# Kernel optimization log

Measured on AMD Instinct MI355X. Metric: run time of the kernel, lower is better.

The kernel has to match this reference:

```python
import jax, jax.numpy as jnp
import numpy as np

N_NODES = 100000
N_EDGES = 1600000
IN_FEATS = 128
N_HIDDEN = 128
OUT_DIM = 32
BN_EPS = 1e-5


def setup_inputs() -> dict:
    key = jax.random.key(0)
    ks = jax.random.split(key, 12)
    s = 0.05  # weight init scale
    return {
        "features": jax.random.normal(ks[0], (N_NODES, IN_FEATS), dtype=jnp.float32),
        "src": jax.random.randint(ks[1], (N_EDGES,), 0, N_NODES),
        "dst": jax.random.randint(ks[2], (N_EDGES,), 0, N_NODES),
        # layer 0: in_feats -> n_hidden
        "Ws0": jax.random.normal(ks[3], (IN_FEATS, N_HIDDEN), dtype=jnp.float32) * s,
        "Wn0": jax.random.normal(ks[4], (IN_FEATS, N_HIDDEN), dtype=jnp.float32) * s,
        "b0": jnp.zeros((N_HIDDEN,), jnp.float32),
        # layer 1: n_hidden -> n_hidden
        "Ws1": jax.random.normal(ks[5], (N_HIDDEN, N_HIDDEN), dtype=jnp.float32) * s,
        "Wn1": jax.random.normal(ks[6], (N_HIDDEN, N_HIDDEN), dtype=jnp.float32) * s,
        "b1": jnp.zeros((N_HIDDEN,), jnp.float32),
        # layer 2 (output): n_hidden -> out_dim, no activation
        "Ws2": jax.random.normal(ks[7], (N_HIDDEN, OUT_DIM), dtype=jnp.float32) * s,
        "Wn2": jax.random.normal(ks[8], (N_HIDDEN, OUT_DIM), dtype=jnp.float32) * s,
        "b2": jnp.zeros((OUT_DIM,), jnp.float32),
        # batch norms after layers 0 and 1
        "g0": jnp.ones((N_HIDDEN,), jnp.float32),
        "be0": jnp.zeros((N_HIDDEN,), jnp.float32),
        "g1": jnp.ones((N_HIDDEN,), jnp.float32),
        "be1": jnp.zeros((N_HIDDEN,), jnp.float32),
    }


def _sage_mean(h, src, dst, inv_deg, Ws, Wn, b):
    # DGL SAGEConv('mean'): fc_self(h) + fc_neigh(mean of in-neighbor feats)
    agg = jax.ops.segment_sum(h[src], dst, num_segments=N_NODES) * inv_deg
    return h @ Ws + agg @ Wn + b


def _batch_norm(h, gamma, beta):
    mu = jnp.mean(h, axis=0)
    var = jnp.var(h, axis=0)
    return (h - mu) * jax.lax.rsqrt(var + BN_EPS) * gamma + beta


def reference(features, src, dst, Ws0, Wn0, b0, Ws1, Wn1, b1, Ws2, Wn2, b2, g0, be0, g1, be1):
    ones = jnp.ones((N_EDGES,), jnp.float32)
    deg = jax.ops.segment_sum(ones, dst, num_segments=N_NODES)
    inv_deg = (1.0 / jnp.maximum(deg, 1.0))[:, None]  # [N,1]

    # layer 0: SAGEConv internal activation, then BN + external activation
    h = jax.nn.relu(_sage_mean(features, src, dst, inv_deg, Ws0, Wn0, b0))
    h = jax.nn.relu(_batch_norm(h, g0, be0))
    # layer 1 (hidden)
    h = jax.nn.relu(_sage_mean(h, src, dst, inv_deg, Ws1, Wn1, b1))
    h = jax.nn.relu(_batch_norm(h, g1, be1))
    # layer 2 (output): no activation, no BN (idx > n_hidden_layers)
    h = _sage_mean(h, src, dst, inv_deg, Ws2, Wn2, b2)

    # dgl.mean_nodes over a single graph -> [1, out_dim], then softmax over classes
    hg = jnp.mean(h, axis=0, keepdims=True)
    return jax.nn.softmax(hg, axis=1)
```

## Files before the change

### kernel.cpp

```cpp
#include <hip/hip_runtime.h>
#include <hip/hip_bf16.h>

typedef __hip_bfloat16 bf16;
typedef __hip_bfloat162 bf162;

#define NN 100000
#define NE 1600000
#define BN_EPS 1e-5f

#define BSH 8
#define NBUCK ((NN + 255) >> BSH)
#define ABLK 128
#define EPBA ((NE + ABLK - 1) / ABLK)
#define CAP 6144

struct alignas(16) bf16x8 { bf16 v[8]; };

typedef __bf16 bfrag __attribute__((ext_vector_type(8)));
typedef float f4 __attribute__((ext_vector_type(4)));
typedef float f2 __attribute__((ext_vector_type(2)));

static __device__ __forceinline__ float b2f(bf16 x){ return __bfloat162float(x); }
static __device__ __forceinline__ bf16 f2b(float x){ return __float2bfloat16(x); }

static __device__ __forceinline__ uint2 pk8_fp8(float x0,float x1,float x2,float x3,
                                                float x4,float x5,float x6,float x7)
{
    int lo = __builtin_amdgcn_cvt_pk_fp8_f32(x0, x1, 0, 0);
    lo = __builtin_amdgcn_cvt_pk_fp8_f32(x2, x3, lo, 1);
    int hi = __builtin_amdgcn_cvt_pk_fp8_f32(x4, x5, 0, 0);
    hi = __builtin_amdgcn_cvt_pk_fp8_f32(x6, x7, hi, 1);
    return make_uint2((unsigned)lo, (unsigned)hi);
}

__global__ __launch_bounds__(256) void k_convert(const float* __restrict__ in,
                                                 unsigned char* __restrict__ outf8, int n)
{
    int i = (blockIdx.x * 256 + threadIdx.x) * 8;
    if (i + 7 < n) {
        float4 a = *(const float4*)(in + i);
        float4 b = *(const float4*)(in + i + 4);
        *(uint2*)(outf8 + i) = pk8_fp8(a.x,a.y,a.z,a.w,b.x,b.y,b.z,b.w);
    }
}

__global__ __launch_bounds__(256) void k_wtrans(const float* __restrict__ W0, const float* __restrict__ W1,
                                                const float* __restrict__ W2, const float* __restrict__ W3,
                                                bf16* __restrict__ T0, bf16* __restrict__ T1,
                                                bf16* __restrict__ T2, bf16* __restrict__ T3)
{
    int m = blockIdx.x >> 6;
    int t = (blockIdx.x & 63) * 256 + threadIdx.x;
    const float* W = (m == 0) ? W0 : (m == 1) ? W1 : (m == 2) ? W2 : W3;
    bf16* T = (m == 0) ? T0 : (m == 1) ? T1 : (m == 2) ? T2 : T3;
    int n = t >> 7, k = t & 127;
    T[n * 128 + k] = f2b(W[k * 128 + n]);
}

__global__ __launch_bounds__(256) void k_pa1(const int* __restrict__ dst, const int* __restrict__ src,
                                             int* __restrict__ bucketCountD, int* __restrict__ blockBaseD,
                                             int* __restrict__ bucketCountS, int* __restrict__ blockBaseS)
{
    __shared__ int histD[NBUCK];
    __shared__ int histS[NBUCK];
    int t = threadIdx.x;
    for (int i = t; i < NBUCK; i += 256) { histD[i] = 0; histS[i] = 0; }
    __syncthreads();
    int e0 = blockIdx.x * EPBA, e1 = min(e0 + EPBA, NE);
    for (int e = e0 + t; e < e1; e += 256) {
        unsigned bd = ((unsigned)dst[e]) >> BSH;
        unsigned bs = ((unsigned)src[e]) >> BSH;
        if (bd < (unsigned)NBUCK) atomicAdd(&histD[bd], 1);
        if (bs < (unsigned)NBUCK) atomicAdd(&histS[bs], 1);
    }
    __syncthreads();
    for (int i = t; i < NBUCK; i += 256) {
        blockBaseD[blockIdx.x * NBUCK + i] = atomicAdd(&bucketCountD[i], histD[i]);
        blockBaseS[blockIdx.x * NBUCK + i] = atomicAdd(&bucketCountS[i], histS[i]);
    }
}

__global__ __launch_bounds__(512) void k_bscan2(const int* __restrict__ cntD, int* __restrict__ startD,
                                                const int* __restrict__ cntS, int* __restrict__ startS)
{
    __shared__ int sd[512];
    const int* cnt = (blockIdx.x == 0) ? cntD : cntS;
    int* start = (blockIdx.x == 0) ? startD : startS;
    int t = threadIdx.x;
    int v = (t < NBUCK) ? cnt[t] : 0;
    sd[t] = v;
    __syncthreads();
    for (int o = 1; o < 512; o <<= 1) {
        int x = (t >= o) ? sd[t - o] : 0;
        __syncthreads();
        sd[t] += x;
        __syncthreads();
    }
    if (t < NBUCK) start[t] = sd[t] - v;
    if (t == 0) start[NBUCK] = NE;
}

__global__ __launch_bounds__(256) void k_pa2(const int* __restrict__ src, const int* __restrict__ dst,
                                             const int* __restrict__ bucketStartD, const int* __restrict__ blockBaseD,
                                             const int* __restrict__ bucketStartS, const int* __restrict__ blockBaseS,
                                             unsigned* __restrict__ packD, unsigned* __restrict__ packS)
{
    __shared__ int baseD[NBUCK];
    __shared__ int curD[NBUCK];
    __shared__ int baseS[NBUCK];
    __shared__ int curS[NBUCK];
    int t = threadIdx.x;
    for (int i = t; i < NBUCK; i += 256) {
        baseD[i] = bucketStartD[i] + blockBaseD[blockIdx.x * NBUCK + i];
        curD[i] = 0;
        baseS[i] = bucketStartS[i] + blockBaseS[blockIdx.x * NBUCK + i];
        curS[i] = 0;
    }
    __syncthreads();
    int e0 = blockIdx.x * EPBA, e1 = min(e0 + EPBA, NE);
    for (int e = e0 + t; e < e1; e += 256) {
        int s = src[e], d = dst[e];
        unsigned bd = ((unsigned)d) >> BSH;
        if (bd < (unsigned)NBUCK) {
            int r = atomicAdd(&curD[bd], 1);
            unsigned idx = (unsigned)(baseD[bd] + r);
            if (idx < (unsigned)NE)
                packD[idx] = (((unsigned)d & 255u) << 24) | ((unsigned)s & 0xFFFFFFu);
        }
        unsigned bs = ((unsigned)s) >> BSH;
        if (bs < (unsigned)NBUCK) {
            int r = atomicAdd(&curS[bs], 1);
            unsigned idx = (unsigned)(baseS[bs] + r);
            if (idx < (unsigned)NE)
                packS[idx] = (((unsigned)s & 255u) << 24) | ((unsigned)d & 0xFFFFFFu);
        }
    }
}

__global__ __launch_bounds__(256) void k_pbD(const unsigned* __restrict__ packD, const int* __restrict__ bucketStartD,
                                             int* __restrict__ offs, float* __restrict__ invd,
                                             int* __restrict__ esrc)
{
    __shared__ int dcnt[256];
    __shared__ int sscan[256];
    __shared__ int cur[256];
    __shared__ int S[CAP];
    int t = threadIdx.x;
    int b = blockIdx.x;
    int base = b << BSH;
    dcnt[t] = 0;
    cur[t] = 0;
    for (int i = t; i < CAP; i += 256) S[i] = 0;
    __syncthreads();
    int p0 = bucketStartD[b], p1 = bucketStartD[b + 1];
    int cnt = p1 - p0;
    for (int i = p0 + t; i < p1; i += 256)
        atomicAdd(&dcnt[packD[i] >> 24], 1);
    __syncthreads();
    int my = dcnt[t];
    sscan[t] = my;
    __syncthreads();
    for (int o = 1; o < 256; o <<= 1) {
        int v = (t >= o) ? sscan[t - o] : 0;
        __syncthreads();
        sscan[t] += v;
        __syncthreads();
    }
    int lo = sscan[t] - my;
    if (base + t < NN) {
        offs[base + t] = p0 + lo;
        invd[base + t] = 1.0f / (float)max(my, 1);
    }
    if (b == NBUCK - 1 && t == 0) offs[NN] = NE;
    __syncthreads();
    sscan[t] = lo;
    __syncthreads();
    if (cnt <= CAP) {
        for (int i = p0 + t; i < p1; i += 256) {
            unsigned v = packD[i];
            unsigned li = v >> 24;
            int pos = sscan[li] + atomicAdd(&cur[li], 1);
            if ((unsigned)pos >= (unsigned)cnt) pos = cnt - 1;
            S[pos] = (int)(v & 0xFFFFFFu);
        }
        __syncthreads();
        for (int i = t; i < cnt; i += 256) esrc[p0 + i] = S[i];
    } else {
        for (int i = p0 + t; i < p1; i += 256) {
            unsigned v = packD[i];
            unsigned li = v >> 24;
            int pos = sscan[li] + atomicAdd(&cur[li], 1);
            if ((unsigned)pos >= (unsigned)cnt) pos = cnt - 1;
            esrc[p0 + pos] = (int)(v & 0xFFFFFFu);
        }
    }
}

__global__ __launch_bounds__(256) void k_wsrc2(const unsigned* __restrict__ packS, const int* __restrict__ bucketStartS,
                                               const float* __restrict__ invd, float* __restrict__ wsrc)
{
    __shared__ float wacc[256];
    int t = threadIdx.x;
    wacc[t] = 0.f;
    __syncthreads();
    int b = blockIdx.x;
    int base = b << BSH;
    int p0 = bucketStartS[b], p1 = bucketStartS[b + 1];
    for (int i = p0 + t; i < p1; i += 256) {
        unsigned v = packS[i];
        unsigned li = v >> 24;
        unsigned dy = v & 0xFFFFFFu;
        if (dy >= (unsigned)NN) dy = 0u;
        atomicAdd(&wacc[li], invd[dy]);
    }
    __syncthreads();
    if (base + t < NN) wsrc[base + t] = wacc[t];
}

__global__ __launch_bounds__(256) void k_aggregate(const unsigned char* __restrict__ inf8, bf16* __restrict__ out,
                                                   const int* __restrict__ offs, const int* __restrict__ esrc,
                                                   const float* __restrict__ invd,
                                                   const float* __restrict__ scsh, int use_ss)
{
    int row = blockIdx.x * 4 + (threadIdx.x >> 6);
    if (row >= NN) return;
    int lane = threadIdx.x & 63;
    int grp = lane >> 4;
    int c0 = (lane & 15) * 8;
    float sc[8], sh[8];
    if (use_ss) {
#pragma unroll
        for (int j = 0; j < 8; j++) { sc[j] = scsh[c0 + j]; sh[j] = scsh[128 + c0 + j]; }
    }
    int e0 = offs[row], e1 = offs[row + 1];
    float a[8];
#pragma unroll
    for (int j = 0; j < 8; j++) a[j] = 0.f;

    auto unpack = [&](uint2 u, float* v) {
        f2 p0 = __builtin_amdgcn_cvt_pk_f32_fp8(u.x, 0);
        f2 p1 = __builtin_amdgcn_cvt_pk_f32_fp8(u.x, 1);
        f2 p2 = __builtin_amdgcn_cvt_pk_f32_fp8(u.y, 0);
        f2 p3 = __builtin_amdgcn_cvt_pk_f32_fp8(u.y, 1);
        v[0]=p0.x; v[1]=p0.y; v[2]=p1.x; v[3]=p1.y; v[4]=p2.x; v[5]=p2.y; v[6]=p3.x; v[7]=p3.y;
    };

    int e = e0 + grp;
    for (; e + 12 < e1; e += 16) {
        int s0 = esrc[e], s1 = esrc[e + 4], s2 = esrc[e + 8], s3 = esrc[e + 12];
        uint2 u0 = *(const uint2*)&inf8[(size_t)s0 * 128 + c0];
        uint2 u1 = *(const uint2*)&inf8[(size_t)s1 * 128 + c0];
        uint2 u2 = *(const uint2*)&inf8[(size_t)s2 * 128 + c0];
        uint2 u3 = *(const uint2*)&inf8[(size_t)s3 * 128 + c0];
        float v0[8], v1[8], v2[8], v3[8];
        unpack(u0, v0); unpack(u1, v1); unpack(u2, v2); unpack(u3, v3);
        if (use_ss) {
#pragma unroll
            for (int j = 0; j < 8; j++)
                a[j] += fmaxf(v0[j] * sc[j] + sh[j], 0.f) + fmaxf(v1[j] * sc[j] + sh[j], 0.f)
                      + fmaxf(v2[j] * sc[j] + sh[j], 0.f) + fmaxf(v3[j] * sc[j] + sh[j], 0.f);
        } else {
#pragma unroll
            for (int j = 0; j < 8; j++)
                a[j] += (v0[j] + v1[j]) + (v2[j] + v3[j]);
        }
    }
    if (e < e1) {
        int i1 = e + 4, i2 = e + 8;
        float m1 = (i1 < e1) ? 1.f : 0.f;
        float m2 = (i2 < e1) ? 1.f : 0.f;
        if (i1 >= e1) i1 = e;
        if (i2 >= e1) i2 = e;
        int s0 = esrc[e], s1 = esrc[i1], s2 = esrc[i2];
        uint2 u0 = *(const uint2*)&inf8[(size_t)s0 * 128 + c0];
        uint2 u1 = *(const uint2*)&inf8[(size_t)s1 * 128 + c0];
        uint2 u2 = *(const uint2*)&inf8[(size_t)s2 * 128 + c0];
        float v0[8], v1[8], v2[8];
        unpack(u0, v0); unpack(u1, v1); unpack(u2, v2);
        if (use_ss) {
#pragma unroll
            for (int j = 0; j < 8; j++)
                a[j] += fmaxf(v0[j] * sc[j] + sh[j], 0.f)
                      + m1 * fmaxf(v1[j] * sc[j] + sh[j], 0.f)
                      + m2 * fmaxf(v2[j] * sc[j] + sh[j], 0.f);
        } else {
#pragma unroll
            for (int j = 0; j < 8; j++)
                a[j] += v0[j] + m1 * v1[j] + m2 * v2[j];
        }
    }
#pragma unroll
    for (int j = 0; j < 8; j++) {
        a[j] += __shfl_xor(a[j], 16);
        a[j] += __shfl_xor(a[j], 32);
    }
    if (grp == 0) {
        float id = invd[row];
        bf16x8 o;
#pragma unroll
        for (int j = 0; j < 8; j++) o.v[j] = f2b(a[j] * id);
        *(bf16x8*)&out[(size_t)row * 128 + c0] = o;
    }
}

#define GM 128
__global__ __launch_bounds__(256) void k_gemm_mfma(const void* __restrict__ HsSrc, int hs_fp8,
                                                   const bf16* __restrict__ Ag,
                                                   const bf16* __restrict__ Wst, const bf16* __restrict__ Wnt,
                                                   const float* __restrict__ bias,
                                                   const float* __restrict__ scsh, int use_ss,
                                                   bf16* __restrict__ outp, unsigned char* __restrict__ outf8,
                                                   float* __restrict__ bnsums)
{
    __shared__ bf16 smem[2][128][72];
    __shared__ float sredsum[128], sredsq[128];
    int t = threadIdx.x;
    int row0 = blockIdx.x * GM;
    int lane = t & 63;
    int l16 = lane & 15;
    int quad = lane >> 4;
    int m0w = (t >> 6) * 32;

    if (t < 128) { sredsum[t] = 0.f; sredsq[t] = 0.f; }

    f4 acc[2][8];
#pragma unroll
    for (int rt = 0; rt < 2; rt++)
#pragma unroll
        for (int ct = 0; ct < 8; ct++) { f4 z = {0.f, 0.f, 0.f, 0.f}; acc[rt][ct] = z; }

    for (int kc = 0; kc < 128; kc += 64) {
#pragma unroll
        for (int i = 0; i < 4; i++) {
            int f = i * 256 + t;
            int row = f >> 3;
            int col8 = (f & 7) * 8;
            int grow = row0 + row;
            float hv32[8];
            bf16x8 av;
            if (grow < NN) {
                if (hs_fp8) {
                    uint2 u = *(const uint2*)((const unsigned char*)HsSrc + (size_t)grow * 128 + kc + col8);
                    f2 q0 = __builtin_amdgcn_cvt_pk_f32_fp8(u.x, 0);
                    f2 q1 = __builtin_amdgcn_cvt_pk_f32_fp8(u.x, 1);
                    f2 q2 = __builtin_amdgcn_cvt_pk_f32_fp8(u.y, 0);
                    f2 q3 = __builtin_amdgcn_cvt_pk_f32_fp8(u.y, 1);
                    hv32[0]=q0.x; hv32[1]=q0.y; hv32[2]=q1.x; hv32[3]=q1.y;
                    hv32[4]=q2.x; hv32[5]=q2.y; hv32[6]=q3.x; hv32[7]=q3.y;
                } else {
                    const float* fp = (const float*)HsSrc + (size_t)grow * 128 + kc + col8;
                    float4 x = *(const float4*)fp;
                    float4 y = *(const float4*)(fp + 4);
                    hv32[0]=x.x; hv32[1]=x.y; hv32[2]=x.z; hv32[3]=x.w;
                    hv32[4]=y.x; hv32[5]=y.y; hv32[6]=y.z; hv32[7]=y.w;
                }
                av = *(const bf16x8*)&Ag[(size_t)grow * 128 + kc + col8];
            } else {
#pragma unroll
                for (int j = 0; j < 8; j++) { hv32[j] = 0.f; av.v[j] = f2b(0.f); }
            }
            if (use_ss) {
#pragma unroll
                for (int j = 0; j < 8; j++) {
                    int k = kc + col8 + j;
                    hv32[j] = fmaxf(hv32[j] * scsh[k] + scsh[128 + k], 0.f);
                }
            }
            bf16x8 hv;
#pragma unroll
            for (int j = 0; j < 8; j++) hv.v[j] = f2b(hv32[j]);
            *(bf16x8*)&smem[0][row][col8] = hv;
            *(bf16x8*)&smem[1][row][col8] = av;
        }
        __syncthreads();
#pragma unroll
        for (int ks2 = 0; ks2 < 2; ks2++) {
            int ko = ks2 * 32 + quad * 8;
            bfrag ah0 = *(const bfrag*)&smem[0][m0w + l16][ko];
            bfrag ah1 = *(const bfrag*)&smem[0][m0w + 16 + l16][ko];
            bfrag aa0 = *(const bfrag*)&smem[1][m0w + l16][ko];
            bfrag aa1 = *(const bfrag*)&smem[1][m0w + 16 + l16][ko];
            int kg = kc + ks2 * 32 + quad * 8;
#pragma unroll
            for (int ct = 0; ct < 8; ct++) {
                bfrag bs  = *(const bfrag*)&Wst[(ct * 16 + l16) * 128 + kg];
                bfrag bnf = *(const bfrag*)&Wnt[(ct * 16 + l16) * 128 + kg];
                acc[0][ct] = __builtin_amdgcn_mfma_f32_16x16x32_bf16(ah0, bs,  acc[0][ct], 0, 0, 0);
                acc[0][ct] = __builtin_amdgcn_mfma_f32_16x16x32_bf16(aa0, bnf, acc[0][ct], 0, 0, 0);
                acc[1][ct] = __builtin_amdgcn_mfma_f32_16x16x32_bf16(ah1, bs,  acc[1][ct], 0, 0, 0);
                acc[1][ct] = __builtin_amdgcn_mfma_f32_16x16x32_bf16(aa1, bnf, acc[1][ct], 0, 0, 0);
            }
        }
        __syncthreads();
    }

    bf16 (*sout)[136] = (bf16(*)[136])&smem[0][0][0];
    float psum[8], psq[8];
#pragma unroll
    for (int ct = 0; ct < 8; ct++) {
        float bv = bias[ct * 16 + l16];
        float s = 0.f, s2 = 0.f;
#pragma unroll
        for (int rt = 0; rt < 2; rt++) {
#pragma unroll
            for (int r = 0; r < 4; r++) {
                int lrow = m0w + rt * 16 + quad * 4 + r;
                float v = fmaxf(acc[rt][ct][r] + bv, 0.f);
                sout[lrow][ct * 16 + l16] = f2b(v);
                if (row0 + lrow < NN) { s += v; s2 += v * v; }
            }
        }
        psum[ct] = s; psq[ct] = s2;
    }
#pragma unroll
    for (int ct = 0; ct < 8; ct++) {
        psum[ct] += __shfl_xor(psum[ct], 16); psum[ct] += __shfl_xor(psum[ct], 32);
        psq[ct]  += __shfl_xor(psq[ct], 16);  psq[ct]  += __shfl_xor(psq[ct], 32);
    }
    if (lane < 16) {
#pragma unroll
        for (int ct = 0; ct < 8; ct++) {
            atomicAdd(&sredsum[ct * 16 + lane], psum[ct]);
            atomicAdd(&sredsq[ct * 16 + lane],  psq[ct]);
        }
    }
    __syncthreads();
#pragma unroll
    for (int i = 0; i < 8; i++) {
        int f = i * 256 + t;
        int row = f >> 4;
        int c16 = f & 15;
        int grow = row0 + row;
        if (grow < NN) {
            bf16x8 ov = *(const bf16x8*)&sout[row][c16 * 8];
            if (outp) *(bf16x8*)&outp[(size_t)grow * 128 + c16 * 8] = ov;
            if (outf8) {
                *(uint2*)&outf8[(size_t)grow * 128 + c16 * 8] =
                    pk8_fp8(b2f(ov.v[0]), b2f(ov.v[1]), b2f(ov.v[2]), b2f(ov.v[3]),
                            b2f(ov.v[4]), b2f(ov.v[5]), b2f(ov.v[6]), b2f(ov.v[7]));
            }
        }
    }
    if (t < 128) {
        atomicAdd(&bnsums[t], sredsum[t]);
        atomicAdd(&bnsums[128 + t], sredsq[t]);
    }
}

__global__ void k_bn_fin(const float* __restrict__ sums, const float* __restrict__ g,
                         const float* __restrict__ be, float* __restrict__ scsh)
{
    int t = threadIdx.x;
    if (t < 128) {
        float mu = sums[t] / (float)NN;
        float var = sums[128 + t] / (float)NN - mu * mu;
        float sc = g[t] * rsqrtf(var + BN_EPS);
        scsh[t] = sc;
        scsh[128 + t] = be[t] - mu * sc;
    }
}

__global__ __launch_bounds__(256) void k_l2_reduce(const bf16* __restrict__ h, const float* __restrict__ scsh,
                                                   const float* __restrict__ wsrc, float* __restrict__ ue)
{
    __shared__ float su[128], se[128];
    int t = threadIdx.x;
    if (t < 128) { su[t] = 0.f; se[t] = 0.f; }
    __syncthreads();
    int c0 = (t & 15) * 8;
    int rof = t >> 4;
    float sc[8], sh[8];
#pragma unroll
    for (int j = 0; j < 8; j++) { sc[j] = scsh[c0 + j]; sh[j] = scsh[128 + c0 + j]; }
    float u[8], es[8];
#pragma unroll
    for (int j = 0; j < 8; j++) { u[j] = 0.f; es[j] = 0.f; }
    int rpb = (NN + gridDim.x - 1) / gridDim.x;
    int r0 = blockIdx.x * rpb;
    int r1 = min(r0 + rpb, NN);
    for (int r = r0 + rof; r < r1; r += 16) {
        bf16x8 v = *(const bf16x8*)&h[(size_t)r * 128 + c0];
        float w = wsrc[r];
#pragma unroll
        for (int j = 0; j < 8; j++) {
            float x = fmaxf(b2f(v.v[j]) * sc[j] + sh[j], 0.f);
            u[j] += x; es[j] += w * x;
        }
    }
#pragma unroll
    for (int j = 0; j < 8; j++) { atomicAdd(&su[c0 + j], u[j]); atomicAdd(&se[c0 + j], es[j]); }
    __syncthreads();
    if (t < 128) { atomicAdd(&ue[t], su[t]); atomicAdd(&ue[128 + t], se[t]); }
}

__global__ void k_final(const float* __restrict__ ue, const float* __restrict__ Ws2,
                        const float* __restrict__ Wn2, const float* __restrict__ b2,
                        float* __restrict__ out)
{
    __shared__ float logit[32];
    int t = threadIdx.x;
    const float inv = 1.0f / (float)NN;
    if (t < 32) {
        float acc = b2[t];
        for (int k = 0; k < 128; k++)
            acc += (ue[k] * inv) * Ws2[k * 32 + t] + (ue[128 + k] * inv) * Wn2[k * 32 + t];
        logit[t] = acc;
    }
    __syncthreads();
    if (t < 32) {
        float m = -1e30f;
        for (int j = 0; j < 32; j++) m = fmaxf(m, logit[j]);
        float s = 0.f;
        for (int j = 0; j < 32; j++) s += expf(logit[j] - m);
        out[t] = expf(logit[t] - m) / s;
    }
}

extern "C" void kernel_launch(void* const* d_in, const int* in_sizes, int n_in,
                              void* d_out, int out_size, void* d_ws, size_t ws_size,
                              hipStream_t stream)
{
    const float* feat = (const float*)d_in[0];
    const int*   src  = (const int*)d_in[1];
    const int*   dst  = (const int*)d_in[2];
    const float* Ws0  = (const float*)d_in[3];
    const float* Wn0  = (const float*)d_in[4];
    const float* b0   = (const float*)d_in[5];
    const float* Ws1  = (const float*)d_in[6];
    const float* Wn1  = (const float*)d_in[7];
    const float* b1   = (const float*)d_in[8];
    const float* Ws2  = (const float*)d_in[9];
    const float* Wn2  = (const float*)d_in[10];
    const float* b2   = (const float*)d_in[11];
    const float* g0   = (const float*)d_in[12];
    const float* be0  = (const float*)d_in[13];
    const float* g1   = (const float*)d_in[14];
    const float* be1  = (const float*)d_in[15];

    char* p = (char*)d_ws;
    auto alloc = [&](size_t b) -> void* {
        void* r = (void*)p;
        p += (b + 255) & ~(size_t)255;
        return r;
    };
    bf16* A      = (bf16*)alloc((size_t)NN * 128 * 2);
    unsigned char* F8 = (unsigned char*)alloc((size_t)NN * 128);
    unsigned* packS = (unsigned*)alloc((size_t)NE * 4);
    int*  esrc   = (int*)alloc((size_t)NE * 4);
    int*  offs   = (int*)alloc((size_t)(NN + 1) * 4);
    float* invd  = (float*)alloc((size_t)NN * 4);
    float* wsrc  = (float*)alloc((size_t)NN * 4);
    char* zstart = p;
    int*  bucketCountD = (int*)alloc((NBUCK + 1) * 4);
    int*  bucketCountS = (int*)alloc((NBUCK + 1) * 4);
    float* bn0   = (float*)alloc(256 * 4);
    float* bn1   = (float*)alloc(256 * 4);
    float* ue    = (float*)alloc(256 * 4);
    size_t zlen = (size_t)(p - zstart);
    float* scsh0 = (float*)alloc(256 * 4);
    float* scsh1 = (float*)alloc(256 * 4);
    bf16* Ws0t   = (bf16*)alloc(16384 * 2);
    bf16* Wn0t   = (bf16*)alloc(16384 * 2);
    bf16* Ws1t   = (bf16*)alloc(16384 * 2);
    bf16* Wn1t   = (bf16*)alloc(16384 * 2);
    int*  bucketStartD = (int*)alloc((NBUCK + 1) * 4);
    int*  bucketStartS = (int*)alloc((NBUCK + 1) * 4);
    int*  blockBaseD   = (int*)alloc((size_t)ABLK * NBUCK * 4);
    int*  blockBaseS   = (int*)alloc((size_t)ABLK * NBUCK * 4);

    unsigned* packD = (unsigned*)A;

    hipMemsetAsync(zstart, 0, zlen, stream);

    const int GB = (NN + GM - 1) / GM;

    k_convert<<<(NN * 128) / (256 * 8), 256, 0, stream>>>(feat, F8, NN * 128);
    k_wtrans<<<256, 256, 0, stream>>>(Ws0, Wn0, Ws1, Wn1, Ws0t, Wn0t, Ws1t, Wn1t);

    k_pa1<<<ABLK, 256, 0, stream>>>(dst, src, bucketCountD, blockBaseD, bucketCountS, blockBaseS);
    k_bscan2<<<2, 512, 0, stream>>>(bucketCountD, bucketStartD, bucketCountS, bucketStartS);
    k_pa2<<<ABLK, 256, 0, stream>>>(src, dst, bucketStartD, blockBaseD, bucketStartS, blockBaseS, packD, packS);
    k_pbD<<<NBUCK, 256, 0, stream>>>(packD, bucketStartD, offs, invd, esrc);
    k_wsrc2<<<NBUCK, 256, 0, stream>>>(packS, bucketStartS, invd, wsrc);

    k_aggregate<<<(NN + 3) / 4, 256, 0, stream>>>(F8, A, offs, esrc, invd, nullptr, 0);
    k_gemm_mfma<<<GB, 256, 0, stream>>>(feat, 0, A, Ws0t, Wn0t, b0, nullptr, 0, nullptr, F8, bn0);
    k_bn_fin<<<1, 128, 0, stream>>>(bn0, g0, be0, scsh0);

    k_aggregate<<<(NN + 3) / 4, 256, 0, stream>>>(F8, A, offs, esrc, invd, scsh0, 1);
    k_gemm_mfma<<<GB, 256, 0, stream>>>(F8, 1, A, Ws1t, Wn1t, b1, scsh0, 1, A, nullptr, bn1);
    k_bn_fin<<<1, 128, 0, stream>>>(bn1, g1, be1, scsh1);

    k_l2_reduce<<<256, 256, 0, stream>>>(A, scsh1, wsrc, ue);
    k_final<<<1, 64, 0, stream>>>(ue, Ws2, Wn2, b2, (float*)d_out);
}
```

Measured before the change: 483.5 us.

## Shrink GEMM row tile to 64 and load full K in one stage

The fused SAGE GEMM kernel now processes 64 rows per block instead of 128, with each wave owning one 16-row MFMA tile. The whole 128-wide K dimension goes into shared memory in one stage, replacing the two 64-wide chunks. All global loads are issued up front before conversion, and out-of-range rows are clamped rather than branched around. This doubles the block count and halves accumulator registers, aiming for better occupancy and memory-level parallelism. The cost is less reuse of each weight fragment loaded from global memory per block, and twice as many per-block BN-statistic atomics.

New measurement: 528.4 us. 1.09x slower.

```diff
diff --git a/kernel.cpp b/kernel.cpp
--- a/kernel.cpp
+++ b/kernel.cpp
@@ -303,7 +303,7 @@
     }
 }
 
-#define GM 128
+#define GM 64
 __global__ __launch_bounds__(256) void k_gemm_mfma(const void* __restrict__ HsSrc, int hs_fp8,
                                                    const bf16* __restrict__ Ag,
                                                    const bf16* __restrict__ Wst, const bf16* __restrict__ Wnt,
@@ -312,87 +312,91 @@
                                                    bf16* __restrict__ outp, unsigned char* __restrict__ outf8,
                                                    float* __restrict__ bnsums)
 {
-    __shared__ bf16 smem[2][128][72];
+    __shared__ bf16 smem[2][64][136];
     __shared__ float sredsum[128], sredsq[128];
     int t = threadIdx.x;
     int row0 = blockIdx.x * GM;
     int lane = t & 63;
     int l16 = lane & 15;
     int quad = lane >> 4;
-    int m0w = (t >> 6) * 32;
+    int m0 = (t >> 6) * 16;
 
     if (t < 128) { sredsum[t] = 0.f; sredsq[t] = 0.f; }
 
-    f4 acc[2][8];
-#pragma unroll
-    for (int rt = 0; rt < 2; rt++)
-#pragma unroll
-        for (int ct = 0; ct < 8; ct++) { f4 z = {0.f, 0.f, 0.f, 0.f}; acc[rt][ct] = z; }
-
-    for (int kc = 0; kc < 128; kc += 64) {
-#pragma unroll
-        for (int i = 0; i < 4; i++) {
-            int f = i * 256 + t;
-            int row = f >> 3;
-            int col8 = (f & 7) * 8;
-            int grow = row0 + row;
-            float hv32[8];
-            bf16x8 av;
-            if (grow < NN) {
-                if (hs_fp8) {
-                    uint2 u = *(const uint2*)((const unsigned char*)HsSrc + (size_t)grow * 128 + kc + col8);
-                    f2 q0 = __builtin_amdgcn_cvt_pk_f32_fp8(u.x, 0);
-                    f2 q1 = __builtin_amdgcn_cvt_pk_f32_fp8(u.x, 1);
-                    f2 q2 = __builtin_amdgcn_cvt_pk_f32_fp8(u.y, 0);
-                    f2 q3 = __builtin_amdgcn_cvt_pk_f32_fp8(u.y, 1);
-                    hv32[0]=q0.x; hv32[1]=q0.y; hv32[2]=q1.x; hv32[3]=q1.y;
-                    hv32[4]=q2.x; hv32[5]=q2.y; hv32[6]=q3.x; hv32[7]=q3.y;
-                } else {
-                    const float* fp = (const float*)HsSrc + (size_t)grow * 128 + kc + col8;
-                    float4 x = *(const float4*)fp;
-                    float4 y = *(const float4*)(fp + 4);
-                    hv32[0]=x.x; hv32[1]=x.y; hv32[2]=x.z; hv32[3]=x.w;
-                    hv32[4]=y.x; hv32[5]=y.y; hv32[6]=y.z; hv32[7]=y.w;
-                }
-                av = *(const bf16x8*)&Ag[(size_t)grow * 128 + kc + col8];
-            } else {
-#pragma unroll
-                for (int j = 0; j < 8; j++) { hv32[j] = 0.f; av.v[j] = f2b(0.f); }
+    f4 acc[8];
+#pragma unroll
+    for (int ct = 0; ct < 8; ct++) { f4 z = {0.f, 0.f, 0.f, 0.f}; acc[ct] = z; }
+
+    float4 x0[4], x1[4];
+    uint2  uu[4];
+    bf16x8 avv[4];
+#pragma unroll
+    for (int i = 0; i < 4; i++) {
+        int f = i * 256 + t;
+        int row = f >> 4;
+        int col8 = (f & 15) * 8;
+        int grow = row0 + row;
+        int gc = (grow < NN) ? grow : 0;
+        if (hs_fp8) {
+            uu[i] = *(const uint2*)((const unsigned char*)HsSrc + (size_t)gc * 128 + col8);
+        } else {
+            const float* fp = (const float*)HsSrc + (size_t)gc * 128 + col8;
+            x0[i] = *(const float4*)fp;
+            x1[i] = *(const float4*)(fp + 4);
+        }
+        avv[i] = *(const bf16x8*)&Ag[(size_t)gc * 128 + col8];
+    }
+#pragma unroll
+    for (int i = 0; i < 4; i++) {
+        int f = i * 256 + t;
+        int row = f >> 4;
+        int col8 = (f & 15) * 8;
+        bool ok = (row0 + row) < NN;
+        float hv32[8];
+        if (hs_fp8) {
+            f2 q0 = __builtin_amdgcn_cvt_pk_f32_fp8(uu[i].x, 0);
+            f2 q1 = __builtin_amdgcn_cvt_pk_f32_fp8(uu[i].x, 1);
+            f2 q2 = __builtin_amdgcn_cvt_pk_f32_fp8(uu[i].y, 0);
+            f2 q3 = __builtin_amdgcn_cvt_pk_f32_fp8(uu[i].y, 1);
+            hv32[0]=q0.x; hv32[1]=q0.y; hv32[2]=q1.x; hv32[3]=q1.y;
+            hv32[4]=q2.x; hv32[5]=q2.y; hv32[6]=q3.x; hv32[7]=q3.y;
+        } else {
+            hv32[0]=x0[i].x; hv32[1]=x0[i].y; hv32[2]=x0[i].z; hv32[3]=x0[i].w;
+            hv32[4]=x1[i].x; hv32[5]=x1[i].y; hv32[6]=x1[i].z; hv32[7]=x1[i].w;
+        }
+        if (use_ss) {
+#pragma unroll
+            for (int j = 0; j < 8; j++) {
+                int k = col8 + j;
+                hv32[j] = fmaxf(hv32[j] * scsh[k] + scsh[128 + k], 0.f);
             }
-            if (use_ss) {
-#pragma unroll
-                for (int j = 0; j < 8; j++) {
-                    int k = kc + col8 + j;
-                    hv32[j] = fmaxf(hv32[j] * scsh[k] + scsh[128 + k], 0.f);
-                }
-            }
-            bf16x8 hv;
-#pragma unroll
-            for (int j = 0; j < 8; j++) hv.v[j] = f2b(hv32[j]);
-            *(bf16x8*)&smem[0][row][col8] = hv;
-            *(bf16x8*)&smem[1][row][col8] = av;
-        }
-        __syncthreads();
-#pragma unroll
-        for (int ks2 = 0; ks2 < 2; ks2++) {
-            int ko = ks2 * 32 + quad * 8;
-            bfrag ah0 = *(const bfrag*)&smem[0][m0w + l16][ko];
-            bfrag ah1 = *(const bfrag*)&smem[0][m0w + 16 + l16][ko];
-            bfrag aa0 = *(const bfrag*)&smem[1][m0w + l16][ko];
-            bfrag aa1 = *(const bfrag*)&smem[1][m0w + 16 + l16][ko];
-            int kg = kc + ks2 * 32 + quad * 8;
-#pragma unroll
-            for (int ct = 0; ct < 8; ct++) {
-                bfrag bs  = *(const bfrag*)&Wst[(ct * 16 + l16) * 128 + kg];
-                bfrag bnf = *(const bfrag*)&Wnt[(ct * 16 + l16) * 128 + kg];
-                acc[0][ct] = __builtin_amdgcn_mfma_f32_16x16x32_bf16(ah0, bs,  acc[0][ct], 0, 0, 0);
-                acc[0][ct] = __builtin_amdgcn_mfma_f32_16x16x32_bf16(aa0, bnf, acc[0][ct], 0, 0, 0);
-                acc[1][ct] = __builtin_amdgcn_mfma_f32_16x16x32_bf16(ah1, bs,  acc[1][ct], 0, 0, 0);
-                acc[1][ct] = __builtin_amdgcn_mfma_f32_16x16x32_bf16(aa1, bnf, acc[1][ct], 0, 0, 0);
-            }
-        }
-        __syncthreads();
-    }
+        }
+        bf16x8 hv, av = avv[i];
+        if (!ok) {
+#pragma unroll
+            for (int j = 0; j < 8; j++) { hv32[j] = 0.f; av.v[j] = f2b(0.f); }
+        }
+#pragma unroll
+        for (int j = 0; j < 8; j++) hv.v[j] = f2b(hv32[j]);
+        *(bf16x8*)&smem[0][row][col8] = hv;
+        *(bf16x8*)&smem[1][row][col8] = av;
+    }
+    __syncthreads();
+
+#pragma unroll
+    for (int ks = 0; ks < 4; ks++) {
+        int ko = ks * 32 + quad * 8;
+        bfrag ah = *(const bfrag*)&smem[0][m0 + l16][ko];
+        bfrag aa = *(const bfrag*)&smem[1][m0 + l16][ko];
+#pragma unroll
+        for (int ct = 0; ct < 8; ct++) {
+            bfrag bs  = *(const bfrag*)&Wst[(ct * 16 + l16) * 128 + ko];
+            bfrag bnf = *(const bfrag*)&Wnt[(ct * 16 + l16) * 128 + ko];
+            acc[ct] = __builtin_amdgcn_mfma_f32_16x16x32_bf16(ah, bs,  acc[ct], 0, 0, 0);
+            acc[ct] = __builtin_amdgcn_mfma_f32_16x16x32_bf16(aa, bnf, acc[ct], 0, 0, 0);
+        }
+    }
+    __syncthreads();
 
     bf16 (*sout)[136] = (bf16(*)[136])&smem[0][0][0];
     float psum[8], psq[8];
@@ -401,14 +405,11 @@
         float bv = bias[ct * 16 + l16];
         float s = 0.f, s2 = 0.f;
 #pragma unroll
-        for (int rt = 0; rt < 2; rt++) {
-#pragma unroll
-            for (int r = 0; r < 4; r++) {
-                int lrow = m0w + rt * 16 + quad * 4 + r;
-                float v = fmaxf(acc[rt][ct][r] + bv, 0.f);
-                sout[lrow][ct * 16 + l16] = f2b(v);
-                if (row0 + lrow < NN) { s += v; s2 += v * v; }
-            }
+        for (int r = 0; r < 4; r++) {
+            int lrow = m0 + quad * 4 + r;
+            float v = fmaxf(acc[ct][r] + bv, 0.f);
+            sout[lrow][ct * 16 + l16] = f2b(v);
+            if (row0 + lrow < NN) { s += v; s2 += v * v; }
         }
         psum[ct] = s; psq[ct] = s2;
     }
@@ -426,7 +427,7 @@
     }
     __syncthreads();
 #pragma unroll
-    for (int i = 0; i < 8; i++) {
+    for (int i = 0; i < 4; i++) {
         int f = i * 256 + t;
         int row = f >> 4;
         int c16 = f & 15;
```

## Load GEMM A-fragments straight from global into registers, shrink row tile to 64

Applied to the files above, without the earlier changes.

The self-plus-neighbor GEMM kernel no longer stages the H and aggregated tiles through shared memory. Each wave now loads its own 16-row A fragments directly from global memory into registers, with the BN scale/shift applied using vectorized loads. The row tile drops from 128 to 64 rows per block, a launch-bounds occupancy hint of 4 blocks is added, and the output write-back becomes per-wave so a block-wide barrier is removed. This saves LDS traffic and barriers and raises occupancy, at the cost of less reuse of the weight fragments per block, which roughly doubles global weight reads.

After: 512.9 us. 6.1% more time.

```diff
diff --git a/kernel.cpp b/kernel.cpp
--- a/kernel.cpp
+++ b/kernel.cpp
@@ -303,112 +303,112 @@
     }
 }
 
-#define GM 128
-__global__ __launch_bounds__(256) void k_gemm_mfma(const void* __restrict__ HsSrc, int hs_fp8,
-                                                   const bf16* __restrict__ Ag,
-                                                   const bf16* __restrict__ Wst, const bf16* __restrict__ Wnt,
-                                                   const float* __restrict__ bias,
-                                                   const float* __restrict__ scsh, int use_ss,
-                                                   bf16* __restrict__ outp, unsigned char* __restrict__ outf8,
-                                                   float* __restrict__ bnsums)
-{
-    __shared__ bf16 smem[2][128][72];
+#define GM 64
+__global__ __launch_bounds__(256, 4) void k_gemm_mfma(const void* __restrict__ HsSrc, int hs_fp8,
+                                                      const bf16* __restrict__ Ag,
+                                                      const bf16* __restrict__ Wst, const bf16* __restrict__ Wnt,
+                                                      const float* __restrict__ bias,
+                                                      const float* __restrict__ scsh, int use_ss,
+                                                      bf16* __restrict__ outp, unsigned char* __restrict__ outf8,
+                                                      float* __restrict__ bnsums)
+{
+    __shared__ bf16 sout[64][136];
     __shared__ float sredsum[128], sredsq[128];
     int t = threadIdx.x;
-    int row0 = blockIdx.x * GM;
     int lane = t & 63;
     int l16 = lane & 15;
     int quad = lane >> 4;
-    int m0w = (t >> 6) * 32;
+    int m0 = (t >> 6) * 16;
+    int row0 = blockIdx.x * GM;
 
     if (t < 128) { sredsum[t] = 0.f; sredsq[t] = 0.f; }
-
-    f4 acc[2][8];
-#pragma unroll
-    for (int rt = 0; rt < 2; rt++)
-#pragma unroll
-        for (int ct = 0; ct < 8; ct++) { f4 z = {0.f, 0.f, 0.f, 0.f}; acc[rt][ct] = z; }
-
-    for (int kc = 0; kc < 128; kc += 64) {
-#pragma unroll
-        for (int i = 0; i < 4; i++) {
-            int f = i * 256 + t;
-            int row = f >> 3;
-            int col8 = (f & 7) * 8;
-            int grow = row0 + row;
-            float hv32[8];
-            bf16x8 av;
-            if (grow < NN) {
-                if (hs_fp8) {
-                    uint2 u = *(const uint2*)((const unsigned char*)HsSrc + (size_t)grow * 128 + kc + col8);
-                    f2 q0 = __builtin_amdgcn_cvt_pk_f32_fp8(u.x, 0);
-                    f2 q1 = __builtin_amdgcn_cvt_pk_f32_fp8(u.x, 1);
-                    f2 q2 = __builtin_amdgcn_cvt_pk_f32_fp8(u.y, 0);
-                    f2 q3 = __builtin_amdgcn_cvt_pk_f32_fp8(u.y, 1);
-                    hv32[0]=q0.x; hv32[1]=q0.y; hv32[2]=q1.x; hv32[3]=q1.y;
-                    hv32[4]=q2.x; hv32[5]=q2.y; hv32[6]=q3.x; hv32[7]=q3.y;
-                } else {
-                    const float* fp = (const float*)HsSrc + (size_t)grow * 128 + kc + col8;
-                    float4 x = *(const float4*)fp;
-                    float4 y = *(const float4*)(fp + 4);
-                    hv32[0]=x.x; hv32[1]=x.y; hv32[2]=x.z; hv32[3]=x.w;
-                    hv32[4]=y.x; hv32[5]=y.y; hv32[6]=y.z; hv32[7]=y.w;
-                }
-                av = *(const bf16x8*)&Ag[(size_t)grow * 128 + kc + col8];
-            } else {
-#pragma unroll
-                for (int j = 0; j < 8; j++) { hv32[j] = 0.f; av.v[j] = f2b(0.f); }
+    __syncthreads();
+
+    int arow = row0 + m0 + l16;
+    int gc = (arow < NN) ? arow : 0;
+
+    bfrag ah[4], aa[4];
+#pragma unroll
+    for (int ks = 0; ks < 4; ks++)
+        aa[ks] = *(const bfrag*)&Ag[(size_t)gc * 128 + ks * 32 + quad * 8];
+
+    if (hs_fp8) {
+#pragma unroll
+        for (int ks = 0; ks < 4; ks++) {
+            int k0 = ks * 32 + quad * 8;
+            uint2 u = *(const uint2*)((const unsigned char*)HsSrc + (size_t)gc * 128 + k0);
+            f2 q0 = __builtin_amdgcn_cvt_pk_f32_fp8(u.x, 0);
+            f2 q1 = __builtin_amdgcn_cvt_pk_f32_fp8(u.x, 1);
+            f2 q2 = __builtin_amdgcn_cvt_pk_f32_fp8(u.y, 0);
+            f2 q3 = __builtin_amdgcn_cvt_pk_f32_fp8(u.y, 1);
+            float hv[8] = {q0.x,q0.y,q1.x,q1.y,q2.x,q2.y,q3.x,q3.y};
+            if (use_ss) {
+                float4 s0 = *(const float4*)&scsh[k0];
+                float4 s1 = *(const float4*)&scsh[k0 + 4];
+                float4 h0 = *(const float4*)&scsh[128 + k0];
+                float4 h1 = *(const float4*)&scsh[128 + k0 + 4];
+                hv[0] = fmaxf(hv[0]*s0.x + h0.x, 0.f); hv[1] = fmaxf(hv[1]*s0.y + h0.y, 0.f);
+                hv[2] = fmaxf(hv[2]*s0.z + h0.z, 0.f); hv[3] = fmaxf(hv[3]*s0.w + h0.w, 0.f);
+                hv[4] = fmaxf(hv[4]*s1.x + h1.x, 0.f); hv[5] = fmaxf(hv[5]*s1.y + h1.y, 0.f);
+                hv[6] = fmaxf(hv[6]*s1.z + h1.z, 0.f); hv[7] = fmaxf(hv[7]*s1.w + h1.w, 0.f);
             }
+            bfrag f;
+#pragma unroll
+            for (int j = 0; j < 8; j++) f[j] = (__bf16)hv[j];
+            ah[ks] = f;
+        }
+    } else {
+#pragma unroll
+        for (int ks = 0; ks < 4; ks++) {
+            int k0 = ks * 32 + quad * 8;
+            const float* fp = (const float*)HsSrc + (size_t)gc * 128 + k0;
+            float4 x = *(const float4*)fp;
+            float4 y = *(const float4*)(fp + 4);
+            float hv[8] = {x.x,x.y,x.z,x.w,y.x,y.y,y.z,y.w};
             if (use_ss) {
-#pragma unroll
-                for (int j = 0; j < 8; j++) {
-                    int k = kc + col8 + j;
-                    hv32[j] = fmaxf(hv32[j] * scsh[k] + scsh[128 + k], 0.f);
-                }
+                float4 s0 = *(const float4*)&scsh[k0];
+                float4 s1 = *(const float4*)&scsh[k0 + 4];
+                float4 h0 = *(const float4*)&scsh[128 + k0];
+                float4 h1 = *(const float4*)&scsh[128 + k0 + 4];
+                hv[0] = fmaxf(hv[0]*s0.x + h0.x, 0.f); hv[1] = fmaxf(hv[1]*s0.y + h0.y, 0.f);
+                hv[2] = fmaxf(hv[2]*s0.z + h0.z, 0.f); hv[3] = fmaxf(hv[3]*s0.w + h0.w, 0.f);
+                hv[4] = fmaxf(hv[4]*s1.x + h1.x, 0.f); hv[5] = fmaxf(hv[5]*s1.y + h1.y, 0.f);
+                hv[6] = fmaxf(hv[6]*s1.z + h1.z, 0.f); hv[7] = fmaxf(hv[7]*s1.w + h1.w, 0.f);
             }
-            bf16x8 hv;
-#pragma unroll
-            for (int j = 0; j < 8; j++) hv.v[j] = f2b(hv32[j]);
-            *(bf16x8*)&smem[0][row][col8] = hv;
-            *(bf16x8*)&smem[1][row][col8] = av;
-        }
-        __syncthreads();
-#pragma unroll
-        for (int ks2 = 0; ks2 < 2; ks2++) {
-            int ko = ks2 * 32 + quad * 8;
-            bfrag ah0 = *(const bfrag*)&smem[0][m0w + l16][ko];
-            bfrag ah1 = *(const bfrag*)&smem[0][m0w + 16 + l16][ko];
-            bfrag aa0 = *(const bfrag*)&smem[1][m0w + l16][ko];
-            bfrag aa1 = *(const bfrag*)&smem[1][m0w + 16 + l16][ko];
-            int kg = kc + ks2 * 32 + quad * 8;
-#pragma unroll
-            for (int ct = 0; ct < 8; ct++) {
-                bfrag bs  = *(const bfrag*)&Wst[(ct * 16 + l16) * 128 + kg];
-                bfrag bnf = *(const bfrag*)&Wnt[(ct * 16 + l16) * 128 + kg];
-                acc[0][ct] = __builtin_amdgcn_mfma_f32_16x16x32_bf16(ah0, bs,  acc[0][ct], 0, 0, 0);
-                acc[0][ct] = __builtin_amdgcn_mfma_f32_16x16x32_bf16(aa0, bnf, acc[0][ct], 0, 0, 0);
-                acc[1][ct] = __builtin_amdgcn_mfma_f32_16x16x32_bf16(ah1, bs,  acc[1][ct], 0, 0, 0);
-                acc[1][ct] = __builtin_amdgcn_mfma_f32_16x16x32_bf16(aa1, bnf, acc[1][ct], 0, 0, 0);
-            }
-        }
-        __syncthreads();
-    }
-
-    bf16 (*sout)[136] = (bf16(*)[136])&smem[0][0][0];
+            bfrag f;
+#pragma unroll
+            for (int j = 0; j < 8; j++) f[j] = (__bf16)hv[j];
+            ah[ks] = f;
+        }
+    }
+
+    f4 acc[8];
+#pragma unroll
+    for (int ct = 0; ct < 8; ct++) { f4 z = {0.f, 0.f, 0.f, 0.f}; acc[ct] = z; }
+
+#pragma unroll
+    for (int ks = 0; ks < 4; ks++) {
+        int kg = ks * 32 + quad * 8;
+#pragma unroll
+        for (int ct = 0; ct < 8; ct++) {
+            bfrag bs  = *(const bfrag*)&Wst[(ct * 16 + l16) * 128 + kg];
+            bfrag bnf = *(const bfrag*)&Wnt[(ct * 16 + l16) * 128 + kg];
+            acc[ct] = __builtin_amdgcn_mfma_f32_16x16x32_bf16(ah[ks], bs,  acc[ct], 0, 0, 0);
+            acc[ct] = __builtin_amdgcn_mfma_f32_16x16x32_bf16(aa[ks], bnf, acc[ct], 0, 0, 0);
+        }
+    }
+
     float psum[8], psq[8];
 #pragma unroll
     for (int ct = 0; ct < 8; ct++) {
         float bv = bias[ct * 16 + l16];
         float s = 0.f, s2 = 0.f;
 #pragma unroll
-        for (int rt = 0; rt < 2; rt++) {
-#pragma unroll
-            for (int r = 0; r < 4; r++) {
-                int lrow = m0w + rt * 16 + quad * 4 + r;
-                float v = fmaxf(acc[rt][ct][r] + bv, 0.f);
-                sout[lrow][ct * 16 + l16] = f2b(v);
-                if (row0 + lrow < NN) { s += v; s2 += v * v; }
-            }
+        for (int r = 0; r < 4; r++) {
+            int lrow = m0 + quad * 4 + r;
+            float v = fmaxf(acc[ct][r] + bv, 0.f);
+            sout[lrow][ct * 16 + l16] = f2b(v);
+            if (row0 + lrow < NN) { s += v; s2 += v * v; }
         }
         psum[ct] = s; psq[ct] = s2;
     }
@@ -424,12 +424,12 @@
             atomicAdd(&sredsq[ct * 16 + lane],  psq[ct]);
         }
     }
-    __syncthreads();
-#pragma unroll
-    for (int i = 0; i < 8; i++) {
-        int f = i * 256 + t;
-        int row = f >> 4;
-        int c16 = f & 15;
+
+#pragma unroll
+    for (int i = 0; i < 4; i++) {
+        int idx = i * 64 + lane;
+        int row = m0 + (idx >> 4);
+        int c16 = idx & 15;
         int grow = row0 + row;
         if (grow < NN) {
             bf16x8 ov = *(const bf16x8*)&sout[row][c16 * 8];
@@ -441,6 +441,8 @@
             }
         }
     }
+
+    __syncthreads();
     if (t < 128) {
         atomicAdd(&bnsums[t], sredsum[t]);
         atomicAdd(&bnsums[128 + t], sredsq[t]);
```
